# Kernel tuning notes

Measured on AMD Instinct MI355X. Metric: run time of the kernel, lower is better.

Reference implementation:

```python
import jax, jax.numpy as jnp
import numpy as np

EPS = 1e-5
H, W, C, NCLS = 8, 16, 64, 8

def _bn_params(key, c):
    k1, k2, k3, k4 = jax.random.split(key, 4)
    gamma = jax.random.uniform(k1, (c,), minval=0.5, maxval=1.5)
    beta = 0.1 * jax.random.normal(k2, (c,))
    mean = 0.1 * jax.random.normal(k3, (c,))
    var = jax.random.uniform(k4, (c,), minval=0.5, maxval=1.5)
    return jnp.stack([gamma, beta, mean, var]).astype(jnp.float32)  # (4, c)

def bn2d(x, p):
    # eval-mode BatchNorm2d; p: (4, C); x: (B, C, H, W)
    g, b, m, v = p[0], p[1], p[2], p[3]
    s = g * jax.lax.rsqrt(v + EPS)
    return x * s[None, :, None, None] + (b - m * s)[None, :, None, None]

def bn1d_scalar(x, p):
    # eval-mode BatchNorm1d with 1 channel; p: (4, 1); x: (B, 1, F)
    g, b, m, v = p[0], p[1], p[2], p[3]
    s = g * jax.lax.rsqrt(v + EPS)
    return x * s + (b - m * s)

def conv_same(x, w, b):
    y = jax.lax.conv_general_dilated(x, w, (1, 1), 'SAME',
                                     dimension_numbers=('NCHW', 'OIHW', 'NCHW'))
    return y + b[None, :, None, None]

def setup_inputs() -> dict:
    key = jax.random.key(0)
    ks = jax.random.split(key, 24)
    B = 8192
    d = {}
    d['x'] = jax.random.normal(ks[0], (B, 1, H, W), dtype=jnp.float32)
    d['bn0'] = _bn_params(ks[1], 1)
    d['conv1_w'] = 0.1 * jax.random.normal(ks[2], (C, 1, 3, 3), dtype=jnp.float32)
    d['conv1_b'] = jnp.zeros((C,), jnp.float32)
    d['bn1'] = _bn_params(ks[3], C)
    d['conv2_w'] = (0.1 / np.sqrt(C)) * jax.random.normal(ks[4], (C, C, 3, 3), dtype=jnp.float32)
    d['conv2_b'] = jnp.zeros((C,), jnp.float32)
    d['bn2'] = _bn_params(ks[5], C)
    # LocallyConnected2d, kernel_size=1 -> per-pixel (out_c, in_c) weights
    d['lc3_w'] = (1.0 / np.sqrt(C)) * jax.random.normal(ks[6], (C, C, H, W), dtype=jnp.float32)
    d['bn3'] = _bn_params(ks[7], C)
    d['lc4_w'] = (1.0 / np.sqrt(C)) * jax.random.normal(ks[8], (C, C, H, W), dtype=jnp.float32)
    d['bn4'] = _bn_params(ks[9], C)
    F5 = H * W * C
    d['fc5_w'] = (1.0 / np.sqrt(F5)) * jax.random.normal(ks[10], (512, F5), dtype=jnp.float32)
    d['fc5_b'] = jnp.zeros((512,), jnp.float32)
    d['bn5'] = _bn_params(ks[11], 1)
    d['fc6_w'] = (1.0 / np.sqrt(512)) * jax.random.normal(ks[12], (512, 512), dtype=jnp.float32)
    d['fc6_b'] = jnp.zeros((512,), jnp.float32)
    d['bn6'] = _bn_params(ks[13], 1)
    d['fc7_w'] = (1.0 / np.sqrt(512)) * jax.random.normal(ks[14], (128, 512), dtype=jnp.float32)
    d['fc7_b'] = jnp.zeros((128,), jnp.float32)
    d['bn7'] = _bn_params(ks[15], 1)
    d['fc8_w'] = (1.0 / np.sqrt(128)) * jax.random.normal(ks[16], (NCLS, 128), dtype=jnp.float32)
    d['fc8_b'] = jnp.zeros((NCLS,), jnp.float32)
    return d

def reference(x, bn0, conv1_w, conv1_b, bn1, conv2_w, conv2_b, bn2,
              lc3_w, bn3, lc4_w, bn4, fc5_w, fc5_b, bn5,
              fc6_w, fc6_b, bn6, fc7_w, fc7_b, bn7, fc8_w, fc8_b):
    B = x.shape[0]
    # squeeze -> view(B, 16, 8) -> transpose(1,2) -> add channel dim
    h = jnp.swapaxes(x.reshape(B, W, H), 1, 2)[:, None]  # (B,1,H,W)
    h = bn2d(h, bn0)
    h = jax.nn.relu(bn2d(conv_same(h, conv1_w, conv1_b), bn1))
    h = jax.nn.relu(bn2d(conv_same(h, conv2_w, conv2_b), bn2))
    # locally connected, k=1: per-pixel channel mixing
    h = jax.nn.relu(bn2d(jnp.einsum('bchw,ochw->bohw', h, lc3_w), bn3))
    h = jax.nn.relu(bn2d(jnp.einsum('bchw,ochw->bohw', h, lc4_w), bn4))
    h = h.reshape(B, 1, -1)  # (B, 1, C*H*W)
    h = h @ fc5_w.T + fc5_b
    h = jax.nn.relu(bn1d_scalar(h, bn5))
    h = jax.nn.relu(bn1d_scalar(h @ fc6_w.T + fc6_b, bn6))
    h = jax.nn.relu(bn1d_scalar(h @ fc7_w.T + fc7_b, bn7))
    h = h @ fc8_w.T + fc8_b
    return h.reshape(B, NCLS)
```

## Files before the change

### kernel.cpp

```cpp
#include <hip/hip_runtime.h>

typedef unsigned short bf16_t;
typedef __attribute__((ext_vector_type(8))) short bf16x8;
typedef __attribute__((ext_vector_type(8))) unsigned short u16x8;
typedef __attribute__((ext_vector_type(4))) float f32x4;

#if defined(__has_builtin)
#if __has_builtin(__builtin_amdgcn_global_load_lds)
#define HAS_GLL 1
#endif
#endif

__device__ __forceinline__ float b2f(bf16_t u) {
    return __uint_as_float(((unsigned int)u) << 16);
}
__device__ __forceinline__ bf16_t f2b(float f) {
    unsigned int x = __float_as_uint(f);
    unsigned int r = x + 0x7fffu + ((x >> 16) & 1u);
    return (bf16_t)(r >> 16);
}
__device__ __forceinline__ float ldf(const void* p, int i, int isf) {
    return isf ? ((const float*)p)[i] : b2f(((const bf16_t*)p)[i]);
}

__device__ __forceinline__ void stg16(const bf16_t* g, bf16_t* l) {
#ifdef HAS_GLL
    __builtin_amdgcn_global_load_lds(
        (const __attribute__((address_space(1))) unsigned int*)g,
        (__attribute__((address_space(3))) unsigned int*)l,
        16, 0, 0);
#else
    *(uint4*)l = *(const uint4*)g;
#endif
}

#define OFF_S0T0 0
#define OFF_W1   16
#define OFF_S1   592
#define OFF_H1   656
#define OFF_S2   720
#define OFF_H2   784
#define OFF_S3   848
#define OFF_H3   912
#define OFF_S4   976
#define OFF_H4   1040
#define OFF_SC5  1104
#define OFF_H5   1112
#define OFF_SC6  1624
#define OFF_H6   1632
#define OFF_SC7  2144
#define OFF_H7   2152
#define OFF_W8   2280
#define OFF_B8   3304
#define OFF_FLAG 4032

__global__ void detect_kernel(const void* xraw, float* prm)
{
    if (threadIdx.x == 0 && blockIdx.x == 0) {
        const unsigned int* w = (const unsigned int*)xraw;
        int good = 0;
        for (int i = 0; i < 64; i++) {
            float f = __uint_as_float(w[i] << 16);
            float a = fabsf(f);
            if (a >= 0.0009765625f && a <= 16.0f) good++;
        }
        prm[OFF_FLAG] = (good >= 32) ? 0.0f : 1.0f;
    }
}

__global__ __launch_bounds__(256) void cvtb_kernel(
    const void* __restrict__ src, bf16_t* __restrict__ dst, int n,
    const float* __restrict__ prm)
{
    const int isf = prm[OFF_FLAG] > 0.5f;
    int i = blockIdx.x * 256 + threadIdx.x;
    if (i < n) dst[i] = isf ? f2b(((const float*)src)[i]) : ((const bf16_t*)src)[i];
}

__global__ __launch_bounds__(256) void pw2_kernel(
    const void* __restrict__ src, bf16_t* __restrict__ dst,
    const float* __restrict__ prm)
{
    const int isf = prm[OFF_FLAG] > 0.5f;
    int i = blockIdx.x * 256 + threadIdx.x;
    if (i >= 36864) return;
    int oc = i / 576, r = i - oc * 576;
    int tap = r >> 6, ic = r & 63;
    dst[i] = f2b(ldf(src, oc * 576 + ic * 9 + tap, isf));
}

__global__ __launch_bounds__(256) void pw34_kernel(
    const void* __restrict__ src, bf16_t* __restrict__ dst,
    const float* __restrict__ prm)
{
    const int isf = prm[OFF_FLAG] > 0.5f;
    int i = blockIdx.x * 256 + threadIdx.x;
    if (i >= 524288) return;
    int p = i >> 12, r = i & 4095;
    int oc = r >> 6, ic = r & 63;
    dst[i] = f2b(ldf(src, oc * 8192 + ic * 128 + p, isf));
}

__global__ __launch_bounds__(256) void pw5_kernel(
    const void* __restrict__ src, bf16_t* __restrict__ dst,
    const float* __restrict__ prm)
{
    const int isf = prm[OFF_FLAG] > 0.5f;
    int i = blockIdx.x * 256 + threadIdx.x;
    if (i >= 4194304) return;
    int nr = i >> 13, r = i & 8191;
    int p = r >> 6, c = r & 63;
    dst[i] = f2b(ldf(src, nr * 8192 + c * 128 + p, isf));
}

__global__ __launch_bounds__(256) void fold_params_kernel(
    const void* bn0p, const void* w1, const void* b1, const void* bn1p,
    const void* b2c, const void* bn2p, const void* bn3p, const void* bn4p,
    const void* b5, const void* bn5p, const void* b6, const void* bn6p,
    const void* b7, const void* bn7p, const void* w8, const void* b8,
    float* prm)
{
    const int isf = prm[OFF_FLAG] > 0.5f;
    const int t = threadIdx.x;

    if (t == 0) {
        float g = ldf(bn0p, 0, isf), be = ldf(bn0p, 1, isf);
        float m = ldf(bn0p, 2, isf), v = ldf(bn0p, 3, isf);
        float s = g * rsqrtf(v + 1e-5f);
        prm[OFF_S0T0] = s; prm[OFF_S0T0 + 1] = be - m * s;
    }
    for (int i = t; i < 576; i += 256) prm[OFF_W1 + i] = ldf(w1, i, isf);

    if (t < 64) {
        {
            float g = ldf(bn1p, t, isf), be = ldf(bn1p, 64 + t, isf);
            float m = ldf(bn1p, 128 + t, isf), v = ldf(bn1p, 192 + t, isf);
            float s = g * rsqrtf(v + 1e-5f);
            prm[OFF_S1 + t] = s;
            prm[OFF_H1 + t] = s * ldf(b1, t, isf) + (be - m * s);
        }
        {
            float g = ldf(bn2p, t, isf), be = ldf(bn2p, 64 + t, isf);
            float m = ldf(bn2p, 128 + t, isf), v = ldf(bn2p, 192 + t, isf);
            float s = g * rsqrtf(v + 1e-5f);
            prm[OFF_S2 + t] = s;
            prm[OFF_H2 + t] = s * ldf(b2c, t, isf) + (be - m * s);
        }
        {
            float g = ldf(bn3p, t, isf), be = ldf(bn3p, 64 + t, isf);
            float m = ldf(bn3p, 128 + t, isf), v = ldf(bn3p, 192 + t, isf);
            float s = g * rsqrtf(v + 1e-5f);
            prm[OFF_S3 + t] = s;
            prm[OFF_H3 + t] = be - m * s;
        }
        {
            float g = ldf(bn4p, t, isf), be = ldf(bn4p, 64 + t, isf);
            float m = ldf(bn4p, 128 + t, isf), v = ldf(bn4p, 192 + t, isf);
            float s = g * rsqrtf(v + 1e-5f);
            prm[OFF_S4 + t] = s;
            prm[OFF_H4 + t] = be - m * s;
        }
    }
    {
        float g = ldf(bn5p, 0, isf), be = ldf(bn5p, 1, isf);
        float m = ldf(bn5p, 2, isf), v = ldf(bn5p, 3, isf);
        float s = g * rsqrtf(v + 1e-5f);
        if (t == 0) prm[OFF_SC5] = s;
        for (int i = t; i < 512; i += 256)
            prm[OFF_H5 + i] = s * ldf(b5, i, isf) + (be - m * s);
    }
    {
        float g = ldf(bn6p, 0, isf), be = ldf(bn6p, 1, isf);
        float m = ldf(bn6p, 2, isf), v = ldf(bn6p, 3, isf);
        float s = g * rsqrtf(v + 1e-5f);
        if (t == 0) prm[OFF_SC6] = s;
        for (int i = t; i < 512; i += 256)
            prm[OFF_H6 + i] = s * ldf(b6, i, isf) + (be - m * s);
    }
    {
        float g = ldf(bn7p, 0, isf), be = ldf(bn7p, 1, isf);
        float m = ldf(bn7p, 2, isf), v = ldf(bn7p, 3, isf);
        float s = g * rsqrtf(v + 1e-5f);
        if (t == 0) prm[OFF_SC7] = s;
        if (t < 128) prm[OFF_H7 + t] = s * ldf(b7, t, isf) + (be - m * s);
    }
    for (int i = t; i < 1024; i += 256) prm[OFF_W8 + i] = ldf(w8, i, isf);
    if (t < 8) prm[OFF_B8 + t] = ldf(b8, t, isf);
}

__global__ __launch_bounds__(256) void conv1_kernel(
    const void* __restrict__ x, const float* __restrict__ prm,
    bf16_t* __restrict__ c1, int Bc, int c0)
{
    __shared__ float xn[180];
    __shared__ float w1s[576];

    const int t = threadIdx.x;
    const int b = blockIdx.x;
    const int isf = prm[OFF_FLAG] > 0.5f;
    const float s0 = prm[OFF_S0T0], t0 = prm[OFF_S0T0 + 1];

    for (int i = t; i < 576; i += 256) w1s[i] = prm[OFF_W1 + i];
    if (t < 180) {
        int row = t / 18, col = t - row * 18;
        float v = 0.f;
        if (row >= 1 && row <= 8 && col >= 1 && col <= 16)
            v = s0 * ldf(x, (c0 + b) * 128 + (col - 1) * 8 + (row - 1), isf) + t0;
        xn[t] = v;
    }
    __syncthreads();

    const int pg  = t & 31;
    const int oc0 = (t >> 5) * 8;

    float s1[8], h1[8];
    #pragma unroll
    for (int j = 0; j < 8; j++) {
        s1[j] = prm[OFF_S1 + oc0 + j];
        h1[j] = prm[OFF_H1 + oc0 + j];
    }
    #pragma unroll
    for (int m = 0; m < 4; m++) {
        int p = pg + 32 * m;
        int h = p >> 4, w = p & 15;
        float r[9];
        #pragma unroll
        for (int dh = 0; dh < 3; dh++)
            #pragma unroll
            for (int dw = 0; dw < 3; dw++)
                r[dh * 3 + dw] = xn[(h + dh) * 18 + (w + dw)];
        u16x8 o;
        #pragma unroll
        for (int j = 0; j < 8; j++) {
            float acc = 0.f;
            #pragma unroll
            for (int k = 0; k < 9; k++) acc += r[k] * w1s[(oc0 + j) * 9 + k];
            o[j] = f2b(fmaxf(s1[j] * acc + h1[j], 0.f));
        }
        *(u16x8*)(c1 + (size_t)p * Bc * 64 + (size_t)b * 64 + oc0) = o;
    }
}

__global__ __launch_bounds__(256) void fused_mfma_kernel(
    const bf16_t* __restrict__ c1, const bf16_t* __restrict__ w2p,
    const bf16_t* __restrict__ w3p, const bf16_t* __restrict__ w4p,
    const float* __restrict__ prm, bf16_t* __restrict__ bufA, int Bc)
{
    __shared__ bf16_t sm[20480];
    __shared__ int tapPP[9];
    __shared__ int tapKB[9];
    __shared__ int tapN;

    const int t    = threadIdx.x;
    const int lane = t & 63;
    const int wv   = t >> 6;
    const int m0   = blockIdx.x * 256;
    const int p    = blockIdx.y;
    const int h    = p >> 4, w = p & 15;

    const int fr = lane & 15;
    const int fg = lane >> 4;
    const int swz4 = (fr >> 1) & 3;
    const int orow = fg * 4;
    const int ocol = fr;

    if (t == 0) {
        int n = 0;
        for (int tap = 0; tap < 9; tap++) {
            int dh = tap / 3 - 1, dw = tap % 3 - 1;
            int hh = h + dh, ww = w + dw;
            if (hh >= 0 && hh < 8 && ww >= 0 && ww < 16) {
                tapPP[n] = hh * 16 + ww;
                tapKB[n] = tap * 64;
                n++;
            }
        }
        tapN = n;
    }
    __syncthreads();
    const int S = tapN * 2;

    const int rA = t >> 2;
    const int gS = (t & 3) ^ ((t >> 3) & 3);

    f32x4 acc[4][4];
    #pragma unroll
    for (int i = 0; i < 4; i++)
        #pragma unroll
        for (int j = 0; j < 4; j++)
            acc[i][j] = (f32x4){0.f, 0.f, 0.f, 0.f};

    {
        {
            const bf16_t* ab = c1 + (size_t)tapPP[0] * Bc * 64 + (size_t)m0 * 64;
            #pragma unroll
            for (int u = 0; u < 4; u++) {
                const int c = t + 256 * u;
                const int row = c >> 2;
                const int g = (c & 3) ^ ((c >> 3) & 3);
                stg16(ab + row * 64 + g * 8, sm + c * 8);
            }
            stg16(w2p + rA * 576 + tapKB[0] + gS * 8, sm + 16384 + t * 8);
        }
        for (int s = 0; s < S; s++) {
            const int cur = s & 1;
            __syncthreads();
            if (s + 1 < S) {
                const int nb = cur ^ 1;
                const int s1 = s + 1;
                const int vt = s1 >> 1, ic0 = (s1 & 1) * 32;
                const bf16_t* ab = c1 + (size_t)tapPP[vt] * Bc * 64 + (size_t)m0 * 64 + ic0;
                #pragma unroll
                for (int u = 0; u < 4; u++) {
                    const int c = t + 256 * u;
                    const int row = c >> 2;
                    const int g = (c & 3) ^ ((c >> 3) & 3);
                    stg16(ab + row * 64 + g * 8, sm + nb * 8192 + c * 8);
                }
                stg16(w2p + rA * 576 + tapKB[vt] + ic0 + gS * 8,
                      sm + 16384 + nb * 2048 + t * 8);
            }
            const bf16_t* Ab = sm + cur * 8192;
            const bf16_t* Bb = sm + 16384 + cur * 2048;
            bf16x8 af[4], bf[4];
            #pragma unroll
            for (int i = 0; i < 4; i++)
                af[i] = *(const bf16x8*)(Ab + ((wv * 64 + i * 16 + fr) * 4 + (fg ^ swz4)) * 8);
            #pragma unroll
            for (int j = 0; j < 4; j++)
                bf[j] = *(const bf16x8*)(Bb + ((j * 16 + fr) * 4 + (fg ^ swz4)) * 8);
            #pragma unroll
            for (int i = 0; i < 4; i++)
                #pragma unroll
                for (int j = 0; j < 4; j++)
                    acc[i][j] = __builtin_amdgcn_mfma_f32_16x16x32_bf16(
                        af[i], bf[j], acc[i][j], 0, 0, 0);
        }
        __syncthreads();
    }

    #pragma unroll
    for (int j = 0; j < 4; j++) {
        const int oc = j * 16 + ocol;
        const float s = prm[OFF_S2 + oc], hh2 = prm[OFF_H2 + oc];
        #pragma unroll
        for (int i = 0; i < 4; i++) {
            const int rb = wv * 64 + i * 16 + orow;
            #pragma unroll
            for (int r = 0; r < 4; r++)
                sm[(rb + r) * 72 + oc] = f2b(fmaxf(s * acc[i][j][r] + hh2, 0.f));
        }
    }
    __syncthreads();

    #pragma unroll
    for (int i = 0; i < 4; i++)
        #pragma unroll
        for (int j = 0; j < 4; j++)
            acc[i][j] = (f32x4){0.f, 0.f, 0.f, 0.f};

    for (int ks = 0; ks < 2; ks++) {
        stg16(w3p + (size_t)p * 4096 + rA * 64 + ks * 32 + gS * 8, sm + 18432 + t * 8);
        __syncthreads();
        bf16x8 af[4], bf[4];
        #pragma unroll
        for (int i = 0; i < 4; i++)
            af[i] = *(const bf16x8*)(sm + (wv * 64 + i * 16 + fr) * 72 + ks * 32 + fg * 8);
        #pragma unroll
        for (int j = 0; j < 4; j++)
            bf[j] = *(const bf16x8*)(sm + 18432 + ((j * 16 + fr) * 4 + (fg ^ swz4)) * 8);
        #pragma unroll
        for (int i = 0; i < 4; i++)
            #pragma unroll
            for (int j = 0; j < 4; j++)
                acc[i][j] = __builtin_amdgcn_mfma_f32_16x16x32_bf16(
                    af[i], bf[j], acc[i][j], 0, 0, 0);
        __syncthreads();
    }

    #pragma unroll
    for (int j = 0; j < 4; j++) {
        const int oc = j * 16 + ocol;
        const float s = prm[OFF_S3 + oc], hh3 = prm[OFF_H3 + oc];
        #pragma unroll
        for (int i = 0; i < 4; i++) {
            const int rb = wv * 64 + i * 16 + orow;
            #pragma unroll
            for (int r = 0; r < 4; r++)
                sm[(rb + r) * 72 + oc] = f2b(fmaxf(s * acc[i][j][r] + hh3, 0.f));
        }
    }
    __syncthreads();

    #pragma unroll
    for (int i = 0; i < 4; i++)
        #pragma unroll
        for (int j = 0; j < 4; j++)
            acc[i][j] = (f32x4){0.f, 0.f, 0.f, 0.f};

    for (int ks = 0; ks < 2; ks++) {
        stg16(w4p + (size_t)p * 4096 + rA * 64 + ks * 32 + gS * 8, sm + 18432 + t * 8);
        __syncthreads();
        bf16x8 af[4], bf[4];
        #pragma unroll
        for (int i = 0; i < 4; i++)
            af[i] = *(const bf16x8*)(sm + (wv * 64 + i * 16 + fr) * 72 + ks * 32 + fg * 8);
        #pragma unroll
        for (int j = 0; j < 4; j++)
            bf[j] = *(const bf16x8*)(sm + 18432 + ((j * 16 + fr) * 4 + (fg ^ swz4)) * 8);
        #pragma unroll
        for (int i = 0; i < 4; i++)
            #pragma unroll
            for (int j = 0; j < 4; j++)
                acc[i][j] = __builtin_amdgcn_mfma_f32_16x16x32_bf16(
                    af[i], bf[j], acc[i][j], 0, 0, 0);
        __syncthreads();
    }

    #pragma unroll
    for (int j = 0; j < 4; j++) {
        const int oc = j * 16 + ocol;
        const float s = prm[OFF_S4 + oc], hh4 = prm[OFF_H4 + oc];
        #pragma unroll
        for (int i = 0; i < 4; i++) {
            const int rb = wv * 64 + i * 16 + orow;
            #pragma unroll
            for (int r = 0; r < 4; r++)
                sm[(rb + r) * 72 + oc] = f2b(fmaxf(s * acc[i][j][r] + hh4, 0.f));
        }
    }
    __syncthreads();

    const int wrow = t >> 3, wc0 = (t & 7) * 8;
    #pragma unroll
    for (int pass = 0; pass < 8; pass++) {
        const int row = wrow + pass * 32;
        *(uint4*)(bufA + (size_t)(m0 + row) * 8192 + p * 64 + wc0) =
            *(const uint4*)(sm + row * 72 + wc0);
    }
}

__global__ __launch_bounds__(256) void gemm_mfma(
    const bf16_t* __restrict__ A, const bf16_t* __restrict__ W,
    const float* __restrict__ prm, int sc_off, int sh_off,
    bf16_t* __restrict__ out, int K, int N)
{
    __shared__ bf16_t sm[24576];
    const int t    = threadIdx.x;
    const int lane = t & 63;
    const int wv   = t >> 6;
    const int wr   = wv >> 1, wc = wv & 1;
    const int m0   = blockIdx.x * 128, n0 = blockIdx.y * 64;

    const int fr = lane & 15;
    const int fg = lane >> 4;
    const int swz8 = fr & 7;

    const bf16_t* srcA[4]; bf16_t* dstA[4];
    #pragma unroll
    for (int u = 0; u < 4; u++) {
        const int c = t + 256 * u;
        const int row = c >> 3;
        const int g = (c & 7) ^ (row & 7);
        srcA[u] = A + (size_t)(m0 + row) * K + g * 8;
        dstA[u] = sm + c * 8;
    }
    const bf16_t* srcB[2]; bf16_t* dstB[2];
    #pragma unroll
    for (int u = 0; u < 2; u++) {
        const int c = t + 256 * u;
        const int row = c >> 3;
        const int g = (c & 7) ^ (row & 7);
        srcB[u] = W + (size_t)(n0 + row) * K + g * 8;
        dstB[u] = sm + 16384 + c * 8;
    }

    f32x4 acc[4][2];
    #pragma unroll
    for (int i = 0; i < 4; i++)
        #pragma unroll
        for (int j = 0; j < 2; j++)
            acc[i][j] = (f32x4){0.f, 0.f, 0.f, 0.f};

    const int KS = K >> 6;

    #pragma unroll
    for (int u = 0; u < 4; u++) stg16(srcA[u], dstA[u]);
    #pragma unroll
    for (int u = 0; u < 2; u++) stg16(srcB[u], dstB[u]);

    for (int ks = 0; ks < KS; ks++) {
        const int cur = ks & 1;
        __syncthreads();
        if (ks + 1 < KS) {
            const int nb = cur ^ 1;
            const int kk = (ks + 1) << 6;
            #pragma unroll
            for (int u = 0; u < 4; u++) stg16(srcA[u] + kk, dstA[u] + nb * 8192);
            #pragma unroll
            for (int u = 0; u < 2; u++) stg16(srcB[u] + kk, dstB[u] + nb * 4096);
        }
        const bf16_t* Ab = sm + cur * 8192;
        const bf16_t* Bb = sm + 16384 + cur * 4096;
        bf16x8 af[4][2], bf2[2][2];
        #pragma unroll
        for (int i = 0; i < 4; i++)
            #pragma unroll
            for (int hh = 0; hh < 2; hh++) {
                const int r = wr * 64 + i * 16 + fr;
                const int g = hh * 4 + fg;
                af[i][hh] = *(const bf16x8*)(Ab + (r * 8 + (g ^ swz8)) * 8);
            }
        #pragma unroll
        for (int j = 0; j < 2; j++)
            #pragma unroll
            for (int hh = 0; hh < 2; hh++) {
                const int r = wc * 32 + j * 16 + fr;
                const int g = hh * 4 + fg;
                bf2[j][hh] = *(const bf16x8*)(Bb + (r * 8 + (g ^ swz8)) * 8);
            }
        #pragma unroll
        for (int hh = 0; hh < 2; hh++)
            #pragma unroll
            for (int i = 0; i < 4; i++)
                #pragma unroll
                for (int j = 0; j < 2; j++)
                    acc[i][j] = __builtin_amdgcn_mfma_f32_16x16x32_bf16(
                        af[i][hh], bf2[j][hh], acc[i][j], 0, 0, 0);
    }

    const float s    = prm[sc_off];
    const int   orow = fg * 4;
    const int   ocol = fr;
    #pragma unroll
    for (int j = 0; j < 2; j++) {
        const int n  = n0 + wc * 32 + j * 16 + ocol;
        const float sh = prm[sh_off + n];
        #pragma unroll
        for (int i = 0; i < 4; i++) {
            const int mb = m0 + wr * 64 + i * 16 + orow;
            #pragma unroll
            for (int r = 0; r < 4; r++) {
                float v = fmaxf(s * acc[i][j][r] + sh, 0.f);
                out[(size_t)(mb + r) * N + n] = f2b(v);
            }
        }
    }
}

__global__ __launch_bounds__(256) void fc8_kernel(
    const bf16_t* __restrict__ h, const float* __restrict__ prm,
    void* __restrict__ out, int c0)
{
    __shared__ float wsm[8 * 129];
    const int t = threadIdx.x;
    for (int i = t; i < 1024; i += 256) {
        int n = i >> 7, k = i & 127;
        wsm[n * 129 + k] = prm[OFF_W8 + i];
    }
    __syncthreads();
    const int isf = prm[OFF_FLAG] > 0.5f;
    const int bl = t >> 3, n = t & 7;
    const int b = c0 + blockIdx.x * 32 + bl;
    const bf16_t* hb = h + (size_t)(blockIdx.x * 32 + bl) * 128;
    float acc = prm[OFF_B8 + n];
    for (int k = 0; k < 128; k++) acc += b2f(hb[k]) * wsm[n * 129 + k];
    if (isf) ((float*)out)[(size_t)b * 8 + n] = acc;
    else     ((bf16_t*)out)[(size_t)b * 8 + n] = f2b(acc);
}

extern "C" void kernel_launch(void* const* d_in, const int* in_sizes, int n_in,
                              void* d_out, int out_size, void* d_ws, size_t ws_size,
                              hipStream_t stream)
{
    const void* x    = d_in[0];
    const void* bn0p = d_in[1];
    const void* w1   = d_in[2];
    const void* b1   = d_in[3];
    const void* bn1p = d_in[4];
    const void* w2   = d_in[5];
    const void* b2c  = d_in[6];
    const void* bn2p = d_in[7];
    const void* w3   = d_in[8];
    const void* bn3p = d_in[9];
    const void* w4   = d_in[10];
    const void* bn4p = d_in[11];
    const void* w5   = d_in[12];
    const void* b5   = d_in[13];
    const void* bn5p = d_in[14];
    const void* w6   = d_in[15];
    const void* b6   = d_in[16];
    const void* bn6p = d_in[17];
    const void* w7   = d_in[18];
    const void* b7   = d_in[19];
    const void* bn7p = d_in[20];
    const void* w8   = d_in[21];
    const void* b8   = d_in[22];

    char* base = (char*)d_ws;
    float*  prm = (float*)(base + 0);
    bf16_t* w2p = (bf16_t*)(base + 16384);
    bf16_t* w3p = (bf16_t*)(base + 90112);
    bf16_t* w4p = (bf16_t*)(base + 1138688);
    bf16_t* w5p = (bf16_t*)(base + 2187264);
    bf16_t* w6b = (bf16_t*)(base + 10575872);
    bf16_t* w7b = (bf16_t*)(base + 11100160);
    char*   acts = base + 11231232;

    const int B = 8192;
    const size_t FIXED = 11231232ull;

    detect_kernel<<<1, 64, 0, stream>>>(x, prm);
    fold_params_kernel<<<1, 256, 0, stream>>>(
        bn0p, w1, b1, bn1p, b2c, bn2p, bn3p, bn4p,
        b5, bn5p, b6, bn6p, b7, bn7p, w8, b8, prm);

    pw2_kernel<<<(36864 + 255) / 256, 256, 0, stream>>>(w2, w2p, prm);
    pw34_kernel<<<(524288 + 255) / 256, 256, 0, stream>>>(w3, w3p, prm);
    pw34_kernel<<<(524288 + 255) / 256, 256, 0, stream>>>(w4, w4p, prm);
    pw5_kernel<<<(4194304 + 255) / 256, 256, 0, stream>>>(w5, w5p, prm);
    cvtb_kernel<<<(262144 + 255) / 256, 256, 0, stream>>>(w6, w6b, 262144, prm);
    cvtb_kernel<<<(65536 + 255) / 256, 256, 0, stream>>>(w7, w7b, 65536, prm);

    const int Bf = 4096;
    const size_t FULL_NEED = FIXED + (size_t)Bf * 16384ull + (size_t)B * 18688ull;

    if (ws_size >= FULL_NEED) {
        bf16_t* c1   = (bf16_t*)acts;
        bf16_t* bufA = c1 + (size_t)Bf * 8192;
        bf16_t* bufC = bufA + (size_t)B * 8192;
        bf16_t* bufD = bufC + (size_t)B * 512;
        bf16_t* bufE = bufD + (size_t)B * 512;

        for (int c0 = 0; c0 < B; c0 += Bf) {
            conv1_kernel<<<Bf, 256, 0, stream>>>(x, prm, c1, Bf, c0);
            fused_mfma_kernel<<<dim3(Bf / 256, 128), 256, 0, stream>>>(
                c1, w2p, w3p, w4p, prm, bufA + (size_t)c0 * 8192, Bf);
        }
        gemm_mfma<<<dim3(B / 128, 8), 256, 0, stream>>>(
            bufA, w5p, prm, OFF_SC5, OFF_H5, bufC, 8192, 512);
        gemm_mfma<<<dim3(B / 128, 8), 256, 0, stream>>>(
            bufC, w6b, prm, OFF_SC6, OFF_H6, bufD, 512, 512);
        gemm_mfma<<<dim3(B / 128, 2), 256, 0, stream>>>(
            bufD, w7b, prm, OFF_SC7, OFF_H7, bufE, 512, 128);
        fc8_kernel<<<B / 32, 256, 0, stream>>>(bufE, prm, d_out, 0);
    } else {
        size_t avail = (ws_size > FIXED) ? (ws_size - FIXED) : 0;
        int Bc = 8192;
        while (Bc > 256 && (size_t)Bc * 35072ull > avail) Bc >>= 1;

        bf16_t* c1   = (bf16_t*)acts;
        bf16_t* bufA = c1 + (size_t)Bc * 8192;
        bf16_t* bufC = bufA + (size_t)Bc * 8192;
        bf16_t* bufD = bufC + (size_t)Bc * 512;
        bf16_t* bufE = bufD + (size_t)Bc * 512;

        for (int c0 = 0; c0 < B; c0 += Bc) {
            conv1_kernel<<<Bc, 256, 0, stream>>>(x, prm, c1, Bc, c0);
            fused_mfma_kernel<<<dim3(Bc / 256, 128), 256, 0, stream>>>(
                c1, w2p, w3p, w4p, prm, bufA, Bc);
            gemm_mfma<<<dim3(Bc / 128, 8), 256, 0, stream>>>(
                bufA, w5p, prm, OFF_SC5, OFF_H5, bufC, 8192, 512);
            gemm_mfma<<<dim3(Bc / 128, 8), 256, 0, stream>>>(
                bufC, w6b, prm, OFF_SC6, OFF_H6, bufD, 512, 512);
            gemm_mfma<<<dim3(Bc / 128, 2), 256, 0, stream>>>(
                bufD, w7b, prm, OFF_SC7, OFF_H7, bufE, 512, 128);
            fc8_kernel<<<Bc / 32, 256, 0, stream>>>(bufE, prm, d_out, c0);
        }
    }
}
```

Before: 462.9 us.

## Compute two adjacent output pixels per block to reuse conv2 input planes

The fused conv2/LC3/LC4 kernel now processes a horizontal pair of pixels per block. Each loaded neighbour input plane feeds both pixels' accumulators, so each block loads up to 12 planes instead of 2×9 and A-tile global traffic drops. In exchange it doubles the accumulator registers (two 4x4 f32x4 sets), which can hurt occupancy. It also halves the grid's y-dimension and runs the LC3/LC4 stages serially per pixel within the block.

```diff
diff --git a/kernel.cpp b/kernel.cpp
--- a/kernel.cpp
+++ b/kernel.cpp
@@ -241,22 +241,24 @@
     }
 }
 
-__global__ __launch_bounds__(256) void fused_mfma_kernel(
+__global__ __launch_bounds__(256) void fused_pair_kernel(
     const bf16_t* __restrict__ c1, const bf16_t* __restrict__ w2p,
     const bf16_t* __restrict__ w3p, const bf16_t* __restrict__ w4p,
     const float* __restrict__ prm, bf16_t* __restrict__ bufA, int Bc)
 {
-    __shared__ bf16_t sm[20480];
-    __shared__ int tapPP[9];
-    __shared__ int tapKB[9];
-    __shared__ int tapN;
+    __shared__ bf16_t sm[24576];
+    __shared__ int planeOff[12];
+    __shared__ int planeT0[12];
+    __shared__ int planeT1[12];
+    __shared__ int planeN;
 
     const int t    = threadIdx.x;
     const int lane = t & 63;
     const int wv   = t >> 6;
     const int m0   = blockIdx.x * 256;
-    const int p    = blockIdx.y;
-    const int h    = p >> 4, w = p & 15;
+    const int py   = blockIdx.y;
+    const int h    = py >> 3, w0 = (py & 7) * 2;
+    const int p0   = h * 16 + w0;
 
     const int fr = lane & 15;
     const int fg = lane >> 4;
@@ -266,66 +268,82 @@
 
     if (t == 0) {
         int n = 0;
-        for (int tap = 0; tap < 9; tap++) {
-            int dh = tap / 3 - 1, dw = tap % 3 - 1;
-            int hh = h + dh, ww = w + dw;
-            if (hh >= 0 && hh < 8 && ww >= 0 && ww < 16) {
-                tapPP[n] = hh * 16 + ww;
-                tapKB[n] = tap * 64;
+        for (int r = h - 1; r <= h + 1; r++) {
+            if (r < 0 || r >= 8) continue;
+            for (int c = w0 - 1; c <= w0 + 2; c++) {
+                if (c < 0 || c >= 16) continue;
+                planeOff[n] = (r * 16 + c) * Bc * 64;
+                int d0 = c - w0;
+                planeT0[n] = (d0 >= -1 && d0 <= 1) ? ((r - h + 1) * 3 + d0 + 1) : -1;
+                int d1 = d0 - 1;
+                planeT1[n] = (d1 >= -1 && d1 <= 1) ? ((r - h + 1) * 3 + d1 + 1) : -1;
                 n++;
             }
         }
-        tapN = n;
+        planeN = n;
     }
     __syncthreads();
-    const int S = tapN * 2;
-
-    const int rA = t >> 2;
+    const int S = planeN * 2;
+
+    const int rB = t >> 2;
     const int gS = (t & 3) ^ ((t >> 3) & 3);
 
-    f32x4 acc[4][4];
+    f32x4 acc0[4][4], acc1[4][4];
     #pragma unroll
     for (int i = 0; i < 4; i++)
         #pragma unroll
-        for (int j = 0; j < 4; j++)
-            acc[i][j] = (f32x4){0.f, 0.f, 0.f, 0.f};
+        for (int j = 0; j < 4; j++) {
+            acc0[i][j] = (f32x4){0.f, 0.f, 0.f, 0.f};
+            acc1[i][j] = (f32x4){0.f, 0.f, 0.f, 0.f};
+        }
 
     {
-        {
-            const bf16_t* ab = c1 + (size_t)tapPP[0] * Bc * 64 + (size_t)m0 * 64;
+        const bf16_t* ab = c1 + (size_t)planeOff[0] + (size_t)m0 * 64;
+        #pragma unroll
+        for (int u = 0; u < 4; u++) {
+            const int c = t + 256 * u;
+            const int row = c >> 2;
+            const int g = (c & 3) ^ ((c >> 3) & 3);
+            stg16(ab + row * 64 + g * 8, sm + c * 8);
+        }
+        const int tt0 = planeT0[0] >= 0 ? planeT0[0] : 0;
+        const int tt1 = planeT1[0] >= 0 ? planeT1[0] : 0;
+        stg16(w2p + rB * 576 + tt0 * 64 + gS * 8, sm + 16384 + t * 8);
+        stg16(w2p + rB * 576 + tt1 * 64 + gS * 8, sm + 16384 + 2048 + t * 8);
+    }
+    for (int s = 0; s < S; s++) {
+        const int cur = s & 1;
+        __syncthreads();
+        if (s + 1 < S) {
+            const int nb = cur ^ 1;
+            const int s1 = s + 1;
+            const int pl = s1 >> 1, ic0 = (s1 & 1) * 32;
+            const bf16_t* ab = c1 + (size_t)planeOff[pl] + (size_t)m0 * 64 + ic0;
             #pragma unroll
             for (int u = 0; u < 4; u++) {
                 const int c = t + 256 * u;
                 const int row = c >> 2;
                 const int g = (c & 3) ^ ((c >> 3) & 3);
-                stg16(ab + row * 64 + g * 8, sm + c * 8);
+                stg16(ab + row * 64 + g * 8, sm + nb * 8192 + c * 8);
             }
-            stg16(w2p + rA * 576 + tapKB[0] + gS * 8, sm + 16384 + t * 8);
-        }
-        for (int s = 0; s < S; s++) {
-            const int cur = s & 1;
-            __syncthreads();
-            if (s + 1 < S) {
-                const int nb = cur ^ 1;
-                const int s1 = s + 1;
-                const int vt = s1 >> 1, ic0 = (s1 & 1) * 32;
-                const bf16_t* ab = c1 + (size_t)tapPP[vt] * Bc * 64 + (size_t)m0 * 64 + ic0;
-                #pragma unroll
-                for (int u = 0; u < 4; u++) {
-                    const int c = t + 256 * u;
-                    const int row = c >> 2;
-                    const int g = (c & 3) ^ ((c >> 3) & 3);
-                    stg16(ab + row * 64 + g * 8, sm + nb * 8192 + c * 8);
-                }
-                stg16(w2p + rA * 576 + tapKB[vt] + ic0 + gS * 8,
-                      sm + 16384 + nb * 2048 + t * 8);
-            }
-            const bf16_t* Ab = sm + cur * 8192;
-            const bf16_t* Bb = sm + 16384 + cur * 2048;
-            bf16x8 af[4], bf[4];
-            #pragma unroll
-            for (int i = 0; i < 4; i++)
-                af[i] = *(const bf16x8*)(Ab + ((wv * 64 + i * 16 + fr) * 4 + (fg ^ swz4)) * 8);
+            const int tt0 = planeT0[pl] >= 0 ? planeT0[pl] : 0;
+            const int tt1 = planeT1[pl] >= 0 ? planeT1[pl] : 0;
+            stg16(w2p + rB * 576 + tt0 * 64 + ic0 + gS * 8,
+                  sm + 16384 + nb * 4096 + t * 8);
+            stg16(w2p + rB * 576 + tt1 * 64 + ic0 + gS * 8,
+                  sm + 16384 + nb * 4096 + 2048 + t * 8);
+        }
+        const bf16_t* Ab = sm + cur * 8192;
+        const bf16_t* Bb = sm + 16384 + cur * 4096;
+        const int pl = s >> 1;
+
+        bf16x8 af[4];
+        #pragma unroll
+        for (int i = 0; i < 4; i++)
+            af[i] = *(const bf16x8*)(Ab + ((wv * 64 + i * 16 + fr) * 4 + (fg ^ swz4)) * 8);
+
+        if (planeT0[pl] >= 0) {
+            bf16x8 bf[4];
             #pragma unroll
             for (int j = 0; j < 4; j++)
                 bf[j] = *(const bf16x8*)(Bb + ((j * 16 + fr) * 4 + (fg ^ swz4)) * 8);
@@ -333,110 +351,130 @@
             for (int i = 0; i < 4; i++)
                 #pragma unroll
                 for (int j = 0; j < 4; j++)
-                    acc[i][j] = __builtin_amdgcn_mfma_f32_16x16x32_bf16(
-                        af[i], bf[j], acc[i][j], 0, 0, 0);
+                    acc0[i][j] = __builtin_amdgcn_mfma_f32_16x16x32_bf16(
+                        af[i], bf[j], acc0[i][j], 0, 0, 0);
+        }
+        if (planeT1[pl] >= 0) {
+            bf16x8 bf[4];
+            #pragma unroll
+            for (int j = 0; j < 4; j++)
+                bf[j] = *(const bf16x8*)(Bb + 2048 + ((j * 16 + fr) * 4 + (fg ^ swz4)) * 8);
+            #pragma unroll
+            for (int i = 0; i < 4; i++)
+                #pragma unroll
+                for (int j = 0; j < 4; j++)
+                    acc1[i][j] = __builtin_amdgcn_mfma_f32_16x16x32_bf16(
+                        af[i], bf[j], acc1[i][j], 0, 0, 0);
+        }
+    }
+    __syncthreads();
+
+    for (int px = 0; px < 2; px++) {
+        const int p = p0 + px;
+
+        #pragma unroll
+        for (int j = 0; j < 4; j++) {
+            const int oc = j * 16 + ocol;
+            const float s = prm[OFF_S2 + oc], hh2 = prm[OFF_H2 + oc];
+            #pragma unroll
+            for (int i = 0; i < 4; i++) {
+                const int rb = wv * 64 + i * 16 + orow;
+                #pragma unroll
+                for (int r = 0; r < 4; r++) {
+                    float v = px ? acc1[i][j][r] : acc0[i][j][r];
+                    sm[(rb + r) * 72 + oc] = f2b(fmaxf(s * v + hh2, 0.f));
+                }
+            }
         }
         __syncthreads();
-    }
-
-    #pragma unroll
-    for (int j = 0; j < 4; j++) {
-        const int oc = j * 16 + ocol;
-        const float s = prm[OFF_S2 + oc], hh2 = prm[OFF_H2 + oc];
-        #pragma unroll
-        for (int i = 0; i < 4; i++) {
-            const int rb = wv * 64 + i * 16 + orow;
-            #pragma unroll
-            for (int r = 0; r < 4; r++)
-                sm[(rb + r) * 72 + oc] = f2b(fmaxf(s * acc[i][j][r] + hh2, 0.f));
-        }
-    }
-    __syncthreads();
-
-    #pragma unroll
-    for (int i = 0; i < 4; i++)
-        #pragma unroll
-        for (int j = 0; j < 4; j++)
-            acc[i][j] = (f32x4){0.f, 0.f, 0.f, 0.f};
-
-    for (int ks = 0; ks < 2; ks++) {
-        stg16(w3p + (size_t)p * 4096 + rA * 64 + ks * 32 + gS * 8, sm + 18432 + t * 8);
+
+        f32x4 la[4][4];
+        #pragma unroll
+        for (int i = 0; i < 4; i++)
+            #pragma unroll
+            for (int j = 0; j < 4; j++)
+                la[i][j] = (f32x4){0.f, 0.f, 0.f, 0.f};
+
+        for (int ks = 0; ks < 2; ks++) {
+            stg16(w3p + (size_t)p * 4096 + rB * 64 + ks * 32 + gS * 8, sm + 18432 + t * 8);
+            __syncthreads();
+            bf16x8 af2[4], bf[4];
+            #pragma unroll
+            for (int i = 0; i < 4; i++)
+                af2[i] = *(const bf16x8*)(sm + (wv * 64 + i * 16 + fr) * 72 + ks * 32 + fg * 8);
+            #pragma unroll
+            for (int j = 0; j < 4; j++)
+                bf[j] = *(const bf16x8*)(sm + 18432 + ((j * 16 + fr) * 4 + (fg ^ swz4)) * 8);
+            #pragma unroll
+            for (int i = 0; i < 4; i++)
+                #pragma unroll
+                for (int j = 0; j < 4; j++)
+                    la[i][j] = __builtin_amdgcn_mfma_f32_16x16x32_bf16(
+                        af2[i], bf[j], la[i][j], 0, 0, 0);
+            __syncthreads();
+        }
+
+        #pragma unroll
+        for (int j = 0; j < 4; j++) {
+            const int oc = j * 16 + ocol;
+            const float s = prm[OFF_S3 + oc], hh3 = prm[OFF_H3 + oc];
+            #pragma unroll
+            for (int i = 0; i < 4; i++) {
+                const int rb = wv * 64 + i * 16 + orow;
+                #pragma unroll
+                for (int r = 0; r < 4; r++)
+                    sm[(rb + r) * 72 + oc] = f2b(fmaxf(s * la[i][j][r] + hh3, 0.f));
+            }
+        }
         __syncthreads();
-        bf16x8 af[4], bf[4];
+
         #pragma unroll
         for (int i = 0; i < 4; i++)
-            af[i] = *(const bf16x8*)(sm + (wv * 64 + i * 16 + fr) * 72 + ks * 32 + fg * 8);
-        #pragma unroll
-        for (int j = 0; j < 4; j++)
-            bf[j] = *(const bf16x8*)(sm + 18432 + ((j * 16 + fr) * 4 + (fg ^ swz4)) * 8);
-        #pragma unroll
-        for (int i = 0; i < 4; i++)
             #pragma unroll
             for (int j = 0; j < 4; j++)
-                acc[i][j] = __builtin_amdgcn_mfma_f32_16x16x32_bf16(
-                    af[i], bf[j], acc[i][j], 0, 0, 0);
+                la[i][j] = (f32x4){0.f, 0.f, 0.f, 0.f};
+
+        for (int ks = 0; ks < 2; ks++) {
+            stg16(w4p + (size_t)p * 4096 + rB * 64 + ks * 32 + gS * 8, sm + 18432 + t * 8);
+            __syncthreads();
+            bf16x8 af2[4], bf[4];
+            #pragma unroll
+            for (int i = 0; i < 4; i++)
+                af2[i] = *(const bf16x8*)(sm + (wv * 64 + i * 16 + fr) * 72 + ks * 32 + fg * 8);
+            #pragma unroll
+            for (int j = 0; j < 4; j++)
+                bf[j] = *(const bf16x8*)(sm + 18432 + ((j * 16 + fr) * 4 + (fg ^ swz4)) * 8);
+            #pragma unroll
+            for (int i = 0; i < 4; i++)
+                #pragma unroll
+                for (int j = 0; j < 4; j++)
+                    la[i][j] = __builtin_amdgcn_mfma_f32_16x16x32_bf16(
+                        af2[i], bf[j], la[i][j], 0, 0, 0);
+            __syncthreads();
+        }
+
+        #pragma unroll
+        for (int j = 0; j < 4; j++) {
+            const int oc = j * 16 + ocol;
+            const float s = prm[OFF_S4 + oc], hh4 = prm[OFF_H4 + oc];
+            #pragma unroll
+            for (int i = 0; i < 4; i++) {
+                const int rb = wv * 64 + i * 16 + orow;
+                #pragma unroll
+                for (int r = 0; r < 4; r++)
+                    sm[(rb + r) * 72 + oc] = f2b(fmaxf(s * la[i][j][r] + hh4, 0.f));
+            }
+        }
         __syncthreads();
-    }
-
-    #pragma unroll
-    for (int j = 0; j < 4; j++) {
-        const int oc = j * 16 + ocol;
-        const float s = prm[OFF_S3 + oc], hh3 = prm[OFF_H3 + oc];
-        #pragma unroll
-        for (int i = 0; i < 4; i++) {
-            const int rb = wv * 64 + i * 16 + orow;
-            #pragma unroll
-            for (int r = 0; r < 4; r++)
-                sm[(rb + r) * 72 + oc] = f2b(fmaxf(s * acc[i][j][r] + hh3, 0.f));
-        }
-    }
-    __syncthreads();
-
-    #pragma unroll
-    for (int i = 0; i < 4; i++)
-        #pragma unroll
-        for (int j = 0; j < 4; j++)
-            acc[i][j] = (f32x4){0.f, 0.f, 0.f, 0.f};
-
-    for (int ks = 0; ks < 2; ks++) {
-        stg16(w4p + (size_t)p * 4096 + rA * 64 + ks * 32 + gS * 8, sm + 18432 + t * 8);
+
+        const int wrow = t >> 3, wc0 = (t & 7) * 8;
+        #pragma unroll
+        for (int pass = 0; pass < 8; pass++) {
+            const int row = wrow + pass * 32;
+            *(uint4*)(bufA + (size_t)(m0 + row) * 8192 + p * 64 + wc0) =
+                *(const uint4*)(sm + row * 72 + wc0);
+        }
         __syncthreads();
-        bf16x8 af[4], bf[4];
-        #pragma unroll
-        for (int i = 0; i < 4; i++)
-            af[i] = *(const bf16x8*)(sm + (wv * 64 + i * 16 + fr) * 72 + ks * 32 + fg * 8);
-        #pragma unroll
-        for (int j = 0; j < 4; j++)
-            bf[j] = *(const bf16x8*)(sm + 18432 + ((j * 16 + fr) * 4 + (fg ^ swz4)) * 8);
-        #pragma unroll
-        for (int i = 0; i < 4; i++)
-            #pragma unroll
-            for (int j = 0; j < 4; j++)
-                acc[i][j] = __builtin_amdgcn_mfma_f32_16x16x32_bf16(
-                    af[i], bf[j], acc[i][j], 0, 0, 0);
-        __syncthreads();
-    }
-
-    #pragma unroll
-    for (int j = 0; j < 4; j++) {
-        const int oc = j * 16 + ocol;
-        const float s = prm[OFF_S4 + oc], hh4 = prm[OFF_H4 + oc];
-        #pragma unroll
-        for (int i = 0; i < 4; i++) {
-            const int rb = wv * 64 + i * 16 + orow;
-            #pragma unroll
-            for (int r = 0; r < 4; r++)
-                sm[(rb + r) * 72 + oc] = f2b(fmaxf(s * acc[i][j][r] + hh4, 0.f));
-        }
-    }
-    __syncthreads();
-
-    const int wrow = t >> 3, wc0 = (t & 7) * 8;
-    #pragma unroll
-    for (int pass = 0; pass < 8; pass++) {
-        const int row = wrow + pass * 32;
-        *(uint4*)(bufA + (size_t)(m0 + row) * 8192 + p * 64 + wc0) =
-            *(const uint4*)(sm + row * 72 + wc0);
     }
 }
 
@@ -634,7 +672,7 @@
 
         for (int c0 = 0; c0 < B; c0 += Bf) {
             conv1_kernel<<<Bf, 256, 0, stream>>>(x, prm, c1, Bf, c0);
-            fused_mfma_kernel<<<dim3(Bf / 256, 128), 256, 0, stream>>>(
+            fused_pair_kernel<<<dim3(Bf / 256, 64), 256, 0, stream>>>(
                 c1, w2p, w3p, w4p, prm, bufA + (size_t)c0 * 8192, Bf);
         }
         gemm_mfma<<<dim3(B / 128, 8), 256, 0, stream>>>(
@@ -657,7 +695,7 @@
 
         for (int c0 = 0; c0 < B; c0 += Bc) {
             conv1_kernel<<<Bc, 256, 0, stream>>>(x, prm, c1, Bc, c0);
-            fused_mfma_kernel<<<dim3(Bc / 256, 128), 256, 0, stream>>>(
+            fused_pair_kernel<<<dim3(Bc / 256, 64), 256, 0, stream>>>(
                 c1, w2p, w3p, w4p, prm, bufA, Bc);
             gemm_mfma<<<dim3(Bc / 128, 8), 256, 0, stream>>>(
                 bufA, w5p, prm, OFF_SC5, OFF_H5, bufC, 8192, 512);
```

Result: slower. 600.1 us (+29.6%).
